# Optimization experiments

Measured on AMD Instinct MI355X. Metric: run time of the kernel, lower is better.

## Reference

```python
import jax, jax.numpy as jnp
import numpy as np
from jax import lax

NPOINT, NSAMPLE, RADIUS = 1024, 32, 0.2
IN_CH, DIM, HEADS = 64, 128, 4


def _fps(xyz, npoint):
    """Farthest point sampling. xyz: [B,N,3] -> idx [B,npoint] (int32)."""
    B, N, _ = xyz.shape

    def step(carry, _):
        dist, farthest = carry
        centroid = jnp.take_along_axis(xyz, farthest[:, None, None], axis=1)  # [B,1,3]
        d = jnp.sum((xyz - centroid) ** 2, axis=-1)                            # [B,N]
        dist = jnp.minimum(dist, d)
        nxt = jnp.argmax(dist, axis=-1).astype(jnp.int32)
        return (dist, nxt), farthest

    init = (jnp.full((B, N), 1e10, xyz.dtype), jnp.zeros((B,), jnp.int32))
    _, idxs = lax.scan(step, init, None, length=npoint)
    return idxs.T  # [B,npoint]


def _ball_query(radius, nsample, xyz, new_xyz):
    """xyz [B,N,3], new_xyz [B,S,3] -> idx [B,S,nsample]."""
    N = xyz.shape[1]
    sqr = jnp.sum((new_xyz[:, :, None, :] - xyz[:, None, :, :]) ** 2, axis=-1)  # [B,S,N]
    idx = jnp.broadcast_to(jnp.arange(N, dtype=jnp.int32), sqr.shape)
    idx = jnp.where(sqr > radius * radius, N, idx)
    idx = jnp.sort(idx, axis=-1)[..., :nsample]
    first = idx[..., :1]  # center itself always within radius -> valid
    return jnp.where(idx == N, first, idx)


_gather = jax.vmap(lambda a, i: a[i])  # a [N,C], i [S,K] -> [S,K,C]


def _forward(xyz, points, Wc, bc, gamma, beta, mean, var, Wq, Wk, Wv, Wo, Wp, bp):
    xyz_n = xyz.transpose(0, 2, 1)    # [B,N,3]
    pts = points.transpose(0, 2, 1)   # [B,N,D]

    fidx = _fps(xyz_n, NPOINT)                                         # [B,S]
    new_xyz = jnp.take_along_axis(xyz_n, fidx[:, :, None], axis=1)     # [B,S,3]
    gidx = _ball_query(RADIUS, NSAMPLE, xyz_n, new_xyz)                # [B,S,K]

    grouped_xyz = _gather(xyz_n, gidx)                                 # [B,S,K,3]
    rel = grouped_xyz - new_xyz[:, :, None, :]
    grouped_pts = _gather(pts, gidx)                                   # [B,S,K,D]
    feat = jnp.concatenate([rel, grouped_pts], axis=-1)                # [B,S,K,3+D]

    # 1x1 Conv2d + BatchNorm (inference form with running stats)
    h = jnp.einsum('bskc,dc->bskd', feat, Wc) + bc
    h = (h - mean) * gamma * lax.rsqrt(var + 1e-5) + beta              # [B,S,K,DIM]

    # local transformer: xyz positional encoding + MHSA over the K neighbors
    pos = jnp.einsum('bskc,cd->bskd', grouped_xyz, Wp) + bp
    x = h + pos
    B, S, K, D = x.shape
    hd = D // HEADS
    q = (x @ Wq).reshape(B, S, K, HEADS, hd)
    k = (x @ Wk).reshape(B, S, K, HEADS, hd)
    v = (x @ Wv).reshape(B, S, K, HEADS, hd)
    attn = jax.nn.softmax(jnp.einsum('bsqhd,bskhd->bshqk', q, k) * (hd ** -0.5), axis=-1)
    o = jnp.einsum('bshqk,bskhd->bsqhd', attn, v).reshape(B, S, K, D)
    out = x + o @ Wo                                                   # [B,S,K,DIM]

    new_points = jnp.max(out, axis=2).transpose(0, 2, 1)               # [B,DIM,S]
    return new_xyz.transpose(0, 2, 1), new_points


def setup_inputs() -> dict:
    key = jax.random.key(0)
    ks = jax.random.split(key, 9)
    C = IN_CH + 3
    s = lambda k, shp: (jax.random.normal(k, shp, jnp.float32) * 0.02)
    return dict(
        xyz=jax.random.uniform(ks[0], (8, 3, 4096), jnp.float32),
        points=jax.random.normal(ks[1], (8, IN_CH, 4096), jnp.float32),
        Wc=s(ks[2], (DIM, C)), bc=jnp.zeros((DIM,), jnp.float32),
        gamma=jnp.ones((DIM,), jnp.float32), beta=jnp.zeros((DIM,), jnp.float32),
        mean=jnp.zeros((DIM,), jnp.float32), var=jnp.ones((DIM,), jnp.float32),
        Wq=s(ks[3], (DIM, DIM)), Wk=s(ks[4], (DIM, DIM)),
        Wv=s(ks[5], (DIM, DIM)), Wo=s(ks[6], (DIM, DIM)),
        Wp=s(ks[7], (3, DIM)), bp=jnp.zeros((DIM,), jnp.float32),
    )


def reference(xyz, points, Wc, bc, gamma, beta, mean, var, Wq, Wk, Wv, Wo, Wp, bp):
    return _forward(xyz, points, Wc, bc, gamma, beta, mean, var, Wq, Wk, Wv, Wo, Wp, bp)
```

## Files before the change

kernel.cpp:

```cpp
#include <hip/hip_runtime.h>
#include <math.h>

#define B 8
#define N 4096
#define S 1024
#define K 32
#define CIN 64
#define DIM 128
#define NH 4
#define HD 32
#define PTROW 68
#define NT_BLOCKS 256

typedef __attribute__((ext_vector_type(8))) short bfrag;
typedef __attribute__((ext_vector_type(4))) float f32x4;

#define MFMA(a, b, c) __builtin_amdgcn_mfma_f32_16x16x32_bf16((a), (b), (c), 0, 0, 0)

__device__ __forceinline__ unsigned short f2bf(float f) {
    union { float f; unsigned u; } v; v.f = f;
    unsigned r = v.u + 0x7FFFu + ((v.u >> 16) & 1u);
    return (unsigned short)(r >> 16);
}

#define DPPMAXF(var, CTRL) {                                                              \
    int _o = __builtin_amdgcn_update_dpp(__float_as_int(var), __float_as_int(var),        \
                                         CTRL, 0xf, 0xf, false);                          \
    var = fmaxf(var, __int_as_float(_o));                                                 \
}
#define DPPMINU(var, CTRL) {                                                              \
    unsigned _o = (unsigned)__builtin_amdgcn_update_dpp((int)(var), (int)(var),           \
                                                        CTRL, 0xf, 0xf, false);          \
    var = (_o < (var)) ? _o : (var);                                                      \
}

__global__ __launch_bounds__(256) void k_mega(
    const float* __restrict__ xyz, const float* __restrict__ points,
    const float* __restrict__ Wc, const float* __restrict__ bc,
    const float* __restrict__ gamma, const float* __restrict__ beta,
    const float* __restrict__ mean, const float* __restrict__ var,
    const float* __restrict__ Wp, const float* __restrict__ bp,
    const float* __restrict__ Wq, const float* __restrict__ Wk,
    const float* __restrict__ Wv, const float* __restrict__ Wo,
    float* __restrict__ ptsT, float* __restrict__ nxyz, float* __restrict__ out_xyz,
    unsigned short* __restrict__ WF, float* __restrict__ biasv) {
    __shared__ float pxyz[N * 3];
    __shared__ float cent[S * 3];
    __shared__ __align__(16) unsigned long long wbuf[2][4];
    const int tid = threadIdx.x;
    int blk = blockIdx.x;

    if (blk < 8) {
        const int b = blk;
        const float* X = xyz + (size_t)b * 3 * N;
        float px[16], py[16], pz[16], pd[16];
#pragma unroll
        for (int i = 0; i < 16; i++) {
            int n = tid + i * 256;
            px[i] = X[n]; py[i] = X[N + n]; pz[i] = X[2 * N + n];
            pxyz[n * 3 + 0] = px[i];
            pxyz[n * 3 + 1] = py[i];
            pxyz[n * 3 + 2] = pz[i];
            pd[i] = 1e10f;
        }
        __syncthreads();
        float cx = pxyz[0], cy = pxyz[1], cz = pxyz[2];

        for (int t = 0; t < S; t++) {
            if (tid == 0) { cent[t * 3] = cx; cent[t * 3 + 1] = cy; cent[t * 3 + 2] = cz; }
            if (t == S - 1) break;

            float bv = -1.0f; int slot = 0;
#pragma unroll
            for (int i = 0; i < 16; i++) {
                float dx = px[i] - cx, dy = py[i] - cy, dz = pz[i] - cz;
                float d = __fadd_rn(__fadd_rn(__fmul_rn(dx, dx), __fmul_rn(dy, dy)), __fmul_rn(dz, dz));
                float pn = fminf(pd[i], d);
                pd[i] = pn;
                bool gt = pn > bv;
                bv = gt ? pn : bv;
                slot = gt ? i : slot;
            }
            float m = bv;
            DPPMAXF(m, 0x111)
            DPPMAXF(m, 0x112)
            DPPMAXF(m, 0x114)
            DPPMAXF(m, 0x118)
            DPPMAXF(m, 0x142)
            DPPMAXF(m, 0x143)
            float wmax = __int_as_float(__builtin_amdgcn_readlane(__float_as_int(m), 63));
            unsigned bi = (unsigned)(tid + (slot << 8));
            unsigned bic = (bv == wmax) ? bi : 0xFFFFFFFFu;
            DPPMINU(bic, 0x111)
            DPPMINU(bic, 0x112)
            DPPMINU(bic, 0x114)
            DPPMINU(bic, 0x118)
            DPPMINU(bic, 0x142)
            DPPMINU(bic, 0x143)
            if ((tid & 63) == 63) {
                unsigned long long key =
                    ((unsigned long long)__float_as_uint(wmax) << 32) | (0xFFFFFFFFu - bic);
                wbuf[t & 1][tid >> 6] = key;
            }
            __syncthreads();
            ulonglong2 ab = *(const ulonglong2*)&wbuf[t & 1][0];
            ulonglong2 cd = *(const ulonglong2*)&wbuf[t & 1][2];
            unsigned long long kA = ab.x > ab.y ? ab.x : ab.y;
            unsigned long long kB = cd.x > cd.y ? cd.x : cd.y;
            unsigned long long km = kA > kB ? kA : kB;
            int best = (int)(0xFFFFFFFFu - (unsigned)km);
            cx = pxyz[best * 3]; cy = pxyz[best * 3 + 1]; cz = pxyz[best * 3 + 2];
        }
        __syncthreads();
        for (int i = tid; i < S; i += 256) {
            float a = cent[i * 3], c1 = cent[i * 3 + 1], c2 = cent[i * 3 + 2];
            nxyz[(b * S + i) * 3 + 0] = a;
            nxyz[(b * S + i) * 3 + 1] = c1;
            nxyz[(b * S + i) * 3 + 2] = c2;
            out_xyz[b * 3 * S + i] = a;
            out_xyz[b * 3 * S + S + i] = c1;
            out_xyz[b * 3 * S + 2 * S + i] = c2;
        }
        return;
    }
    blk -= 8;
    if (blk < NT_BLOCKS) {
        const int total = B * N * PTROW;
        for (int idx = blk * 256 + tid; idx < total; idx += NT_BLOCKS * 256) {
            int c = idx % PTROW;
            int n = (idx / PTROW) % N;
            int b = idx / (PTROW * N);
            float v = 0.0f;
            if (c < 3) v = xyz[(b * 3 + c) * N + n];
            else if (c < 67) v = points[(b * CIN + (c - 3)) * N + n];
            ptsT[idx] = v;
        }
        return;
    }
    blk -= NT_BLOCKS;
    if (blk < 19) {
        int mat, kt, base;
        if (blk < 3) { mat = 0; kt = blk; base = 0; }
        else { mat = 1 + (blk - 3) / 4; kt = (blk - 3) % 4; base = 12288 + (mat - 1) * 16384; }
        const float* W = (mat == 1) ? Wq : (mat == 2) ? Wk : (mat == 3) ? Wv : Wo;
        const int lane = tid & 63;
#pragma unroll
        for (int g2 = 0; g2 < 2; g2++) {
            int gnt = (tid >> 6) * 2 + g2;
            int n = gnt * 16 + (lane & 15);
            int k0 = kt * 32 + (lane >> 4) * 8;
            unsigned short* dst = WF + base + (size_t)((kt * 8 + gnt) * 64 + lane) * 8;
            float a = (mat == 0) ? (gamma[n] / sqrtf(var[n] + 1e-5f)) : 0.0f;
#pragma unroll
            for (int i = 0; i < 8; i++) {
                int k = k0 + i;
                float v;
                if (mat == 0) v = (k < 67) ? Wc[n * 67 + k] * a : (k < 70) ? Wp[(k - 67) * 128 + n] : 0.0f;
                else v = W[k * 128 + n];
                dst[i] = f2bf(v);
            }
        }
        return;
    }
    if (tid < DIM) {
        float a = gamma[tid] / sqrtf(var[tid] + 1e-5f);
        biasv[tid] = bc[tid] * a + beta[tid] - mean[tid] * a + bp[tid];
    }
}

__global__ void k_ball(const float* __restrict__ xyz, const float* __restrict__ nxyz,
                       int* __restrict__ gidx) {
    const int g = blockIdx.x * 4 + (threadIdx.x >> 6);
    const int lane = threadIdx.x & 63;
    const int b = g >> 10;
    const float* X = xyz + (size_t)b * 3 * N;
    float cx = nxyz[g * 3 + 0], cy = nxyz[g * 3 + 1], cz = nxyz[g * 3 + 2];
    int cnt = 0;
    int first = -1;
    for (int base = 0; base < N && cnt < K; base += 64) {
        int n = base + lane;
        float dx = cx - X[n], dy = cy - X[N + n], dz = cz - X[2 * N + n];
        float d = __fadd_rn(__fadd_rn(__fmul_rn(dx, dx), __fmul_rn(dy, dy)), __fmul_rn(dz, dz));
        bool in = (d <= 0.04f);
        unsigned long long m = __ballot(in);
        int pre = __popcll(m & ((1ull << lane) - 1ull));
        if (in && cnt + pre < K) gidx[g * K + cnt + pre] = n;
        if (first < 0 && m) first = base + (int)__ffsll((unsigned long long)m) - 1;
        cnt += __popcll(m);
    }
    if (cnt < K) {
        for (int i = cnt + lane; i < K; i += 64) gidx[g * K + i] = first;
    }
}

#define LDS_X   0
#define LDS_A   8192
#define LDS_K   16384
#define LDS_VT  24576
#define LDS_MISC 38912
#define LDS_TOTAL 39056

#define LDSA_READ(off, row, colb) \
    (*(const bfrag*)(smem + (off) + ((row) << 8) + ((colb) ^ (((row) & 7) << 4))))
#define LDS_ST16(off, row, colb, val) \
    (*(unsigned short*)(smem + (off) + ((row) << 8) + ((colb) ^ (((row) & 7) << 4))) = (val))

__global__ __launch_bounds__(256, 4) void k_group(
    const float* __restrict__ ptsT, const float* __restrict__ nxyz,
    const int* __restrict__ gidx, const unsigned short* __restrict__ WF,
    const float* __restrict__ bias, float* __restrict__ outp) {
    __shared__ __align__(16) char smem[LDS_TOTAL];
    const int g = blockIdx.x, b = g >> 10, s = g & 1023;
    const int tid = threadIdx.x;
    const int w = tid >> 6, l = tid & 63;
    const int lane16 = l & 15, lquad = l >> 4;
    const int ncol = w * 32;

    int* nidx = (int*)(smem + LDS_MISC);
    float* ctr = (float*)(smem + LDS_MISC + 128);

    if (tid < K) nidx[tid] = gidx[g * K + tid];
    if (tid >= 64 && tid < 67) ctr[tid - 64] = nxyz[g * 3 + (tid - 64)];
    for (int i = tid; i < 32 * 32; i += 256) {
        int p = i >> 5, c = 64 + (i & 31);
        LDS_ST16(LDS_A, p, c * 2, (unsigned short)0);
    }
    __syncthreads();

    {
        const int p = tid >> 3, j = tid & 7;
        const float* src = ptsT + (size_t)(b * N + nidx[p]) * PTROW;
        float c0 = ctr[0], c1 = ctr[1], c2 = ctr[2];
        for (int c = j; c < 70; c += 8) {
            float v;
            if (c < 3) v = src[c] - (c == 0 ? c0 : c == 1 ? c1 : c2);
            else if (c < 67) v = src[c];
            else v = src[c - 67];
            LDS_ST16(LDS_A, p, c * 2, f2bf(v));
        }
    }
    __syncthreads();

    f32x4 accx[2][2];
    {
        float bv0 = bias[ncol + lane16], bv1 = bias[ncol + 16 + lane16];
        accx[0][0] = f32x4{bv0, bv0, bv0, bv0}; accx[1][0] = accx[0][0];
        accx[0][1] = f32x4{bv1, bv1, bv1, bv1}; accx[1][1] = accx[0][1];
        const bfrag* WallF = (const bfrag*)WF;
#pragma unroll
        for (int kt = 0; kt < 3; kt++) {
            bfrag a0 = LDSA_READ(LDS_A, lane16, kt * 64 + lquad * 16);
            bfrag a1 = LDSA_READ(LDS_A, 16 + lane16, kt * 64 + lquad * 16);
            bfrag b0 = WallF[(kt * 8 + w * 2 + 0) * 64 + l];
            bfrag b1 = WallF[(kt * 8 + w * 2 + 1) * 64 + l];
            accx[0][0] = MFMA(a0, b0, accx[0][0]);
            accx[0][1] = MFMA(a0, b1, accx[0][1]);
            accx[1][0] = MFMA(a1, b0, accx[1][0]);
            accx[1][1] = MFMA(a1, b1, accx[1][1]);
        }
#pragma unroll
        for (int mt = 0; mt < 2; mt++)
#pragma unroll
            for (int nt = 0; nt < 2; nt++)
#pragma unroll
                for (int r = 0; r < 4; r++)
                    LDS_ST16(LDS_X, mt * 16 + lquad * 4 + r, (ncol + nt * 16 + lane16) * 2,
                             f2bf(accx[mt][nt][r]));
    }
    __syncthreads();

    {
        const bfrag* WQF = (const bfrag*)(WF + 12288);
        const bfrag* WKF = (const bfrag*)(WF + 28672);
        const bfrag* WVF = (const bfrag*)(WF + 45056);
#pragma unroll
        for (int m = 0; m < 3; m++) {
            const bfrag* BW = (m == 0) ? WQF : (m == 1) ? WKF : WVF;
            f32x4 acc[2][2] = {};
#pragma unroll
            for (int kt = 0; kt < 4; kt++) {
                bfrag a0 = LDSA_READ(LDS_X, lane16, kt * 64 + lquad * 16);
                bfrag a1 = LDSA_READ(LDS_X, 16 + lane16, kt * 64 + lquad * 16);
                bfrag b0 = BW[(kt * 8 + w * 2 + 0) * 64 + l];
                bfrag b1 = BW[(kt * 8 + w * 2 + 1) * 64 + l];
                acc[0][0] = MFMA(a0, b0, acc[0][0]);
                acc[0][1] = MFMA(a0, b1, acc[0][1]);
                acc[1][0] = MFMA(a1, b0, acc[1][0]);
                acc[1][1] = MFMA(a1, b1, acc[1][1]);
            }
            if (m < 2) {
                int dst = (m == 0) ? LDS_A : LDS_K;
#pragma unroll
                for (int mt = 0; mt < 2; mt++)
#pragma unroll
                    for (int nt = 0; nt < 2; nt++)
#pragma unroll
                        for (int r = 0; r < 4; r++)
                            LDS_ST16(dst, mt * 16 + lquad * 4 + r, (ncol + nt * 16 + lane16) * 2,
                                     f2bf(acc[mt][nt][r]));
            } else {
#pragma unroll
                for (int mt = 0; mt < 2; mt++)
#pragma unroll
                    for (int nt = 0; nt < 2; nt++)
#pragma unroll
                        for (int r = 0; r < 4; r++) {
                            int d = ncol + nt * 16 + lane16;
                            int j = mt * 16 + lquad * 4 + r;
                            *(unsigned short*)(smem + LDS_VT + d * 112 + j * 2) = f2bf(acc[mt][nt][r]);
                        }
            }
        }
    }
    __syncthreads();

    {
        const int h = w;
        const int hb = h * 64;
        bfrag aq0 = LDSA_READ(LDS_A, lane16, hb + lquad * 16);
        bfrag aq1 = LDSA_READ(LDS_A, 16 + lane16, hb + lquad * 16);
        bfrag bk0 = LDSA_READ(LDS_K, lane16, hb + lquad * 16);
        bfrag bk1 = LDSA_READ(LDS_K, 16 + lane16, hb + lquad * 16);
        f32x4 sc[2][2] = {};
        sc[0][0] = MFMA(aq0, bk0, sc[0][0]);
        sc[0][1] = MFMA(aq0, bk1, sc[0][1]);
        sc[1][0] = MFMA(aq1, bk0, sc[1][0]);
        sc[1][1] = MFMA(aq1, bk1, sc[1][1]);

        const float scale = 0.17677669529663687f;
        float p_[2][2][4];
        float mx[2][4], sm[2][4];
#pragma unroll
        for (int mt = 0; mt < 2; mt++)
#pragma unroll
            for (int r = 0; r < 4; r++) {
                p_[mt][0][r] = sc[mt][0][r] * scale;
                p_[mt][1][r] = sc[mt][1][r] * scale;
                mx[mt][r] = fmaxf(p_[mt][0][r], p_[mt][1][r]);
            }
#pragma unroll
        for (int d = 1; d < 16; d <<= 1)
#pragma unroll
            for (int mt = 0; mt < 2; mt++)
#pragma unroll
                for (int r = 0; r < 4; r++)
                    mx[mt][r] = fmaxf(mx[mt][r], __shfl_xor(mx[mt][r], d));
#pragma unroll
        for (int mt = 0; mt < 2; mt++)
#pragma unroll
            for (int r = 0; r < 4; r++) {
                float e0 = __expf(p_[mt][0][r] - mx[mt][r]);
                float e1 = __expf(p_[mt][1][r] - mx[mt][r]);
                p_[mt][0][r] = e0; p_[mt][1][r] = e1;
                sm[mt][r] = e0 + e1;
            }
#pragma unroll
        for (int d = 1; d < 16; d <<= 1)
#pragma unroll
            for (int mt = 0; mt < 2; mt++)
#pragma unroll
                for (int r = 0; r < 4; r++)
                    sm[mt][r] += __shfl_xor(sm[mt][r], d);
#pragma unroll
        for (int mt = 0; mt < 2; mt++)
#pragma unroll
            for (int r = 0; r < 4; r++) {
                float inv = 1.0f / sm[mt][r];
                int row = mt * 16 + lquad * 4 + r;
                LDS_ST16(LDS_X, row, (h * 32 + lane16) * 2, f2bf(p_[mt][0][r] * inv));
                LDS_ST16(LDS_X, row, (h * 32 + 16 + lane16) * 2, f2bf(p_[mt][1][r] * inv));
            }

        f32x4 oacc[2][2] = {};
        bfrag ap0 = LDSA_READ(LDS_X, lane16, hb + lquad * 16);
        bfrag ap1 = LDSA_READ(LDS_X, 16 + lane16, hb + lquad * 16);
        bfrag bv0 = *(const bfrag*)(smem + LDS_VT + (h * 32 + lane16) * 112 + lquad * 16);
        bfrag bv1 = *(const bfrag*)(smem + LDS_VT + (h * 32 + 16 + lane16) * 112 + lquad * 16);
        oacc[0][0] = MFMA(ap0, bv0, oacc[0][0]);
        oacc[0][1] = MFMA(ap0, bv1, oacc[0][1]);
        oacc[1][0] = MFMA(ap1, bv0, oacc[1][0]);
        oacc[1][1] = MFMA(ap1, bv1, oacc[1][1]);
#pragma unroll
        for (int mt = 0; mt < 2; mt++)
#pragma unroll
            for (int nt = 0; nt < 2; nt++)
#pragma unroll
                for (int r = 0; r < 4; r++)
                    LDS_ST16(LDS_A, mt * 16 + lquad * 4 + r, (h * 32 + nt * 16 + lane16) * 2,
                             f2bf(oacc[mt][nt][r]));
    }
    __syncthreads();

    {
        const bfrag* WOF = (const bfrag*)(WF + 61440);
        f32x4 acc[2][2];
#pragma unroll
        for (int mt = 0; mt < 2; mt++)
#pragma unroll
            for (int nt = 0; nt < 2; nt++) acc[mt][nt] = accx[mt][nt];
#pragma unroll
        for (int kt = 0; kt < 4; kt++) {
            bfrag a0 = LDSA_READ(LDS_A, lane16, kt * 64 + lquad * 16);
            bfrag a1 = LDSA_READ(LDS_A, 16 + lane16, kt * 64 + lquad * 16);
            bfrag b0 = WOF[(kt * 8 + w * 2 + 0) * 64 + l];
            bfrag b1 = WOF[(kt * 8 + w * 2 + 1) * 64 + l];
            acc[0][0] = MFMA(a0, b0, acc[0][0]);
            acc[0][1] = MFMA(a0, b1, acc[0][1]);
            acc[1][0] = MFMA(a1, b0, acc[1][0]);
            acc[1][1] = MFMA(a1, b1, acc[1][1]);
        }
        float mnt[2];
#pragma unroll
        for (int nt = 0; nt < 2; nt++) {
            float m = acc[0][nt][0];
#pragma unroll
            for (int r = 1; r < 4; r++) m = fmaxf(m, acc[0][nt][r]);
#pragma unroll
            for (int r = 0; r < 4; r++) m = fmaxf(m, acc[1][nt][r]);
            m = fmaxf(m, __shfl_xor(m, 16));
            m = fmaxf(m, __shfl_xor(m, 32));
            mnt[nt] = m;
        }
        if (lquad == 0) {
#pragma unroll
            for (int nt = 0; nt < 2; nt++) {
                int d = ncol + nt * 16 + lane16;
                outp[((size_t)b * DIM + d) * S + s] = mnt[nt];
            }
        }
    }
}

extern "C" void kernel_launch(void* const* d_in, const int* in_sizes, int n_in,
                              void* d_out, int out_size, void* d_ws, size_t ws_size,
                              hipStream_t stream) {
    const float* xyz = (const float*)d_in[0];
    const float* points = (const float*)d_in[1];
    const float* Wc = (const float*)d_in[2];
    const float* bc = (const float*)d_in[3];
    const float* gamma = (const float*)d_in[4];
    const float* beta = (const float*)d_in[5];
    const float* mean = (const float*)d_in[6];
    const float* var = (const float*)d_in[7];
    const float* Wq = (const float*)d_in[8];
    const float* Wk = (const float*)d_in[9];
    const float* Wv = (const float*)d_in[10];
    const float* Wo = (const float*)d_in[11];
    const float* Wp = (const float*)d_in[12];
    const float* bp = (const float*)d_in[13];

    float* out_xyz = (float*)d_out;
    float* out_pts = out_xyz + B * 3 * S;

    char* ws = (char*)d_ws;
    float* ptsT = (float*)ws;
    size_t off = (size_t)B * N * PTROW * 4;
    float* nxyz = (float*)(ws + off); off += (size_t)B * S * 3 * 4;
    int* gidxp = (int*)(ws + off); off += (size_t)B * S * K * 4;
    unsigned short* WF = (unsigned short*)(ws + off); off += 77824 * 2;
    float* biasv = (float*)(ws + off); off += DIM * 4;

    k_mega<<<8 + NT_BLOCKS + 19 + 1, 256, 0, stream>>>(
        xyz, points, Wc, bc, gamma, beta, mean, var, Wp, bp, Wq, Wk, Wv, Wo,
        ptsT, nxyz, out_xyz, WF, biasv);
    k_ball<<<B * S / 4, 256, 0, stream>>>(xyz, nxyz, gidxp);
    k_group<<<B * S, 256, 0, stream>>>(ptsT, nxyz, gidxp, WF, biasv, out_pts);
}
```

Baseline: 772.0 us.

## Fuse FPS, ball query and grouping into persistent kernel with streaming flags

Merges the three kernels into one persistent launch. Eight blocks run farthest point sampling and publish centroids in chunks of 16 through release atomics and per-batch flags. The remaining 504 worker blocks first do the transpose and weight packing, meet at a grid-wide barrier, then loop over groups, spinning until their centroid is published. Each worker does the ball query inline, so group processing overlaps with the serial FPS and the gidx round trip disappears. In exchange it relies on every block being co-resident, uses spin-waits, and raises LDS use per block, which can lower occupancy.

```diff
diff --git a/kernel.cpp b/kernel.cpp
--- a/kernel.cpp
+++ b/kernel.cpp
@@ -7,10 +7,8 @@
 #define K 32
 #define CIN 64
 #define DIM 128
-#define NH 4
-#define HD 32
 #define PTROW 68
-#define NT_BLOCKS 256
+#define NWORK 504
 
 typedef __attribute__((ext_vector_type(8))) short bfrag;
 typedef __attribute__((ext_vector_type(4))) float f32x4;
@@ -34,7 +32,19 @@
     var = (_o < (var)) ? _o : (var);                                                      \
 }
 
-__global__ __launch_bounds__(256) void k_mega(
+#define LDS_X   0
+#define LDS_A   8192
+#define LDS_K   16384
+#define LDS_VT  24576
+#define LDS_MISC 38912
+#define SMEM_TOTAL 61952
+
+#define LDSA_READ(off, row, colb) \
+    (*(const bfrag*)(smem + (off) + ((row) << 8) + ((colb) ^ (((row) & 7) << 4))))
+#define LDS_ST16(off, row, colb, val) \
+    (*(unsigned short*)(smem + (off) + ((row) << 8) + ((colb) ^ (((row) & 7) << 4))) = (val))
+
+__global__ __launch_bounds__(256) void k_fused(
     const float* __restrict__ xyz, const float* __restrict__ points,
     const float* __restrict__ Wc, const float* __restrict__ bc,
     const float* __restrict__ gamma, const float* __restrict__ beta,
@@ -42,32 +52,42 @@
     const float* __restrict__ Wp, const float* __restrict__ bp,
     const float* __restrict__ Wq, const float* __restrict__ Wk,
     const float* __restrict__ Wv, const float* __restrict__ Wo,
-    float* __restrict__ ptsT, float* __restrict__ nxyz, float* __restrict__ out_xyz,
-    unsigned short* __restrict__ WF, float* __restrict__ biasv) {
-    __shared__ float pxyz[N * 3];
-    __shared__ float cent[S * 3];
-    __shared__ __align__(16) unsigned long long wbuf[2][4];
+    float* __restrict__ ptsT, float* nxyz, float* __restrict__ out_xyz,
+    unsigned short* __restrict__ WF, float* __restrict__ biasv,
+    int* flags, int* tdone, float* __restrict__ outp) {
+    __shared__ __align__(16) char smem[SMEM_TOTAL];
     const int tid = threadIdx.x;
-    int blk = blockIdx.x;
+    const int blk = blockIdx.x;
 
     if (blk < 8) {
         const int b = blk;
         const float* X = xyz + (size_t)b * 3 * N;
+        float* xs = (float*)smem;
+        float* ys = (float*)(smem + 16384);
+        float* zs = (float*)(smem + 32768);
+        float* cent = (float*)(smem + 49152);
+        unsigned long long* wbuf = (unsigned long long*)(smem + 61440);
+
         float px[16], py[16], pz[16], pd[16];
 #pragma unroll
         for (int i = 0; i < 16; i++) {
             int n = tid + i * 256;
             px[i] = X[n]; py[i] = X[N + n]; pz[i] = X[2 * N + n];
-            pxyz[n * 3 + 0] = px[i];
-            pxyz[n * 3 + 1] = py[i];
-            pxyz[n * 3 + 2] = pz[i];
+            xs[n] = px[i]; ys[n] = py[i]; zs[n] = pz[i];
             pd[i] = 1e10f;
         }
         __syncthreads();
-        float cx = pxyz[0], cy = pxyz[1], cz = pxyz[2];
+        float cx = xs[0], cy = ys[0], cz = zs[0];
 
         for (int t = 0; t < S; t++) {
             if (tid == 0) { cent[t * 3] = cx; cent[t * 3 + 1] = cy; cent[t * 3 + 2] = cz; }
+            const bool pub = (t != 0) && ((t & 15) == 0);
+            if (pub && tid < 48) {
+                int row = t - 16 + tid / 3, c = tid % 3;
+                __hip_atomic_store((unsigned*)&nxyz[((size_t)b * S + row) * 3 + c],
+                                   __float_as_uint(cent[row * 3 + c]),
+                                   __ATOMIC_RELEASE, __HIP_MEMORY_SCOPE_AGENT);
+            }
             if (t == S - 1) break;
 
             float bv = -1.0f; int slot = 0;
@@ -89,44 +109,50 @@
             DPPMAXF(m, 0x142)
             DPPMAXF(m, 0x143)
             float wmax = __int_as_float(__builtin_amdgcn_readlane(__float_as_int(m), 63));
-            unsigned bi = (unsigned)(tid + (slot << 8));
-            unsigned bic = (bv == wmax) ? bi : 0xFFFFFFFFu;
-            DPPMINU(bic, 0x111)
-            DPPMINU(bic, 0x112)
-            DPPMINU(bic, 0x114)
-            DPPMINU(bic, 0x118)
-            DPPMINU(bic, 0x142)
-            DPPMINU(bic, 0x143)
-            if ((tid & 63) == 63) {
-                unsigned long long key =
-                    ((unsigned long long)__float_as_uint(wmax) << 32) | (0xFFFFFFFFu - bic);
-                wbuf[t & 1][tid >> 6] = key;
-            }
+            unsigned cand = (bv == wmax) ? (unsigned)(tid + (slot << 8)) : 0xFFFFFFFFu;
+            DPPMINU(cand, 0x111)
+            DPPMINU(cand, 0x112)
+            DPPMINU(cand, 0x114)
+            DPPMINU(cand, 0x118)
+            DPPMINU(cand, 0x142)
+            DPPMINU(cand, 0x143)
+            if ((tid & 63) == 63)
+                wbuf[(t & 1) * 4 + (tid >> 6)] =
+                    ((unsigned long long)__float_as_uint(wmax) << 32) | (0xFFFFFFFFu - cand);
             __syncthreads();
-            ulonglong2 ab = *(const ulonglong2*)&wbuf[t & 1][0];
-            ulonglong2 cd = *(const ulonglong2*)&wbuf[t & 1][2];
+            if (pub && tid == 0)
+                __hip_atomic_fetch_add(&flags[b], 16, __ATOMIC_RELEASE, __HIP_MEMORY_SCOPE_AGENT);
+            ulonglong2 ab = *(const ulonglong2*)&wbuf[(t & 1) * 4 + 0];
+            ulonglong2 cd = *(const ulonglong2*)&wbuf[(t & 1) * 4 + 2];
             unsigned long long kA = ab.x > ab.y ? ab.x : ab.y;
             unsigned long long kB = cd.x > cd.y ? cd.x : cd.y;
             unsigned long long km = kA > kB ? kA : kB;
             int best = (int)(0xFFFFFFFFu - (unsigned)km);
-            cx = pxyz[best * 3]; cy = pxyz[best * 3 + 1]; cz = pxyz[best * 3 + 2];
-        }
-        __syncthreads();
+            cx = xs[best]; cy = ys[best]; cz = zs[best];
+        }
+        __syncthreads();
+        if (tid < 48) {
+            int row = 1008 + tid / 3, c = tid % 3;
+            __hip_atomic_store((unsigned*)&nxyz[((size_t)b * S + row) * 3 + c],
+                               __float_as_uint(cent[row * 3 + c]),
+                               __ATOMIC_RELEASE, __HIP_MEMORY_SCOPE_AGENT);
+        }
+        __syncthreads();
+        if (tid == 0)
+            __hip_atomic_fetch_add(&flags[b], 16, __ATOMIC_RELEASE, __HIP_MEMORY_SCOPE_AGENT);
         for (int i = tid; i < S; i += 256) {
-            float a = cent[i * 3], c1 = cent[i * 3 + 1], c2 = cent[i * 3 + 2];
-            nxyz[(b * S + i) * 3 + 0] = a;
-            nxyz[(b * S + i) * 3 + 1] = c1;
-            nxyz[(b * S + i) * 3 + 2] = c2;
-            out_xyz[b * 3 * S + i] = a;
-            out_xyz[b * 3 * S + S + i] = c1;
-            out_xyz[b * 3 * S + 2 * S + i] = c2;
+            out_xyz[b * 3 * S + i] = cent[i * 3];
+            out_xyz[b * 3 * S + S + i] = cent[i * 3 + 1];
+            out_xyz[b * 3 * S + 2 * S + i] = cent[i * 3 + 2];
         }
         return;
     }
-    blk -= 8;
-    if (blk < NT_BLOCKS) {
+
+    const int w = blk - 8;
+
+    {
         const int total = B * N * PTROW;
-        for (int idx = blk * 256 + tid; idx < total; idx += NT_BLOCKS * 256) {
+        for (int idx = w * 256 + tid; idx < total; idx += NWORK * 256) {
             int c = idx % PTROW;
             int n = (idx / PTROW) % N;
             int b = idx / (PTROW * N);
@@ -135,297 +161,288 @@
             else if (c < 67) v = points[(b * CIN + (c - 3)) * N + n];
             ptsT[idx] = v;
         }
-        return;
+        if (w < 19) {
+            int mat, kt, base;
+            if (w < 3) { mat = 0; kt = w; base = 0; }
+            else { mat = 1 + (w - 3) / 4; kt = (w - 3) % 4; base = 12288 + (mat - 1) * 16384; }
+            const float* W = (mat == 1) ? Wq : (mat == 2) ? Wk : (mat == 3) ? Wv : Wo;
+            const int lane = tid & 63;
+#pragma unroll
+            for (int g2 = 0; g2 < 2; g2++) {
+                int gnt = (tid >> 6) * 2 + g2;
+                int n = gnt * 16 + (lane & 15);
+                int k0 = kt * 32 + (lane >> 4) * 8;
+                unsigned short* dst = WF + base + (size_t)((kt * 8 + gnt) * 64 + lane) * 8;
+                float a = (mat == 0) ? (gamma[n] / sqrtf(var[n] + 1e-5f)) : 0.0f;
+#pragma unroll
+                for (int i = 0; i < 8; i++) {
+                    int k = k0 + i;
+                    float v;
+                    if (mat == 0) v = (k < 67) ? Wc[n * 67 + k] * a : (k < 70) ? Wp[(k - 67) * 128 + n] : 0.0f;
+                    else v = W[k * 128 + n];
+                    dst[i] = f2bf(v);
+                }
+            }
+        }
+        if (w == 19 && tid < DIM) {
+            float a = gamma[tid] / sqrtf(var[tid] + 1e-5f);
+            biasv[tid] = bc[tid] * a + beta[tid] - mean[tid] * a + bp[tid];
+        }
     }
-    blk -= NT_BLOCKS;
-    if (blk < 19) {
-        int mat, kt, base;
-        if (blk < 3) { mat = 0; kt = blk; base = 0; }
-        else { mat = 1 + (blk - 3) / 4; kt = (blk - 3) % 4; base = 12288 + (mat - 1) * 16384; }
-        const float* W = (mat == 1) ? Wq : (mat == 2) ? Wk : (mat == 3) ? Wv : Wo;
-        const int lane = tid & 63;
-#pragma unroll
-        for (int g2 = 0; g2 < 2; g2++) {
-            int gnt = (tid >> 6) * 2 + g2;
-            int n = gnt * 16 + (lane & 15);
-            int k0 = kt * 32 + (lane >> 4) * 8;
-            unsigned short* dst = WF + base + (size_t)((kt * 8 + gnt) * 64 + lane) * 8;
-            float a = (mat == 0) ? (gamma[n] / sqrtf(var[n] + 1e-5f)) : 0.0f;
-#pragma unroll
-            for (int i = 0; i < 8; i++) {
-                int k = k0 + i;
-                float v;
-                if (mat == 0) v = (k < 67) ? Wc[n * 67 + k] * a : (k < 70) ? Wp[(k - 67) * 128 + n] : 0.0f;
-                else v = W[k * 128 + n];
-                dst[i] = f2bf(v);
-            }
-        }
-        return;
+    __threadfence();
+    __syncthreads();
+    if (tid == 0) {
+        __hip_atomic_fetch_add(tdone, 1, __ATOMIC_RELEASE, __HIP_MEMORY_SCOPE_AGENT);
+        while (__hip_atomic_load(tdone, __ATOMIC_ACQUIRE, __HIP_MEMORY_SCOPE_AGENT) < NWORK)
+            __builtin_amdgcn_s_sleep(2);
     }
-    if (tid < DIM) {
-        float a = gamma[tid] / sqrtf(var[tid] + 1e-5f);
-        biasv[tid] = bc[tid] * a + beta[tid] - mean[tid] * a + bp[tid];
-    }
-}
-
-__global__ void k_ball(const float* __restrict__ xyz, const float* __restrict__ nxyz,
-                       int* __restrict__ gidx) {
-    const int g = blockIdx.x * 4 + (threadIdx.x >> 6);
-    const int lane = threadIdx.x & 63;
-    const int b = g >> 10;
-    const float* X = xyz + (size_t)b * 3 * N;
-    float cx = nxyz[g * 3 + 0], cy = nxyz[g * 3 + 1], cz = nxyz[g * 3 + 2];
-    int cnt = 0;
-    int first = -1;
-    for (int base = 0; base < N && cnt < K; base += 64) {
-        int n = base + lane;
-        float dx = cx - X[n], dy = cy - X[N + n], dz = cz - X[2 * N + n];
-        float d = __fadd_rn(__fadd_rn(__fmul_rn(dx, dx), __fmul_rn(dy, dy)), __fmul_rn(dz, dz));
-        bool in = (d <= 0.04f);
-        unsigned long long m = __ballot(in);
-        int pre = __popcll(m & ((1ull << lane) - 1ull));
-        if (in && cnt + pre < K) gidx[g * K + cnt + pre] = n;
-        if (first < 0 && m) first = base + (int)__ffsll((unsigned long long)m) - 1;
-        cnt += __popcll(m);
-    }
-    if (cnt < K) {
-        for (int i = cnt + lane; i < K; i += 64) gidx[g * K + i] = first;
-    }
-}
-
-#define LDS_X   0
-#define LDS_A   8192
-#define LDS_K   16384
-#define LDS_VT  24576
-#define LDS_MISC 38912
-#define LDS_TOTAL 39056
-
-#define LDSA_READ(off, row, colb) \
-    (*(const bfrag*)(smem + (off) + ((row) << 8) + ((colb) ^ (((row) & 7) << 4))))
-#define LDS_ST16(off, row, colb, val) \
-    (*(unsigned short*)(smem + (off) + ((row) << 8) + ((colb) ^ (((row) & 7) << 4))) = (val))
-
-__global__ __launch_bounds__(256, 4) void k_group(
-    const float* __restrict__ ptsT, const float* __restrict__ nxyz,
-    const int* __restrict__ gidx, const unsigned short* __restrict__ WF,
-    const float* __restrict__ bias, float* __restrict__ outp) {
-    __shared__ __align__(16) char smem[LDS_TOTAL];
-    const int g = blockIdx.x, b = g >> 10, s = g & 1023;
-    const int tid = threadIdx.x;
-    const int w = tid >> 6, l = tid & 63;
+    __syncthreads();
+
+    const int wv = tid >> 6, l = tid & 63;
     const int lane16 = l & 15, lquad = l >> 4;
-    const int ncol = w * 32;
-
+    const int ncol = wv * 32;
     int* nidx = (int*)(smem + LDS_MISC);
     float* ctr = (float*)(smem + LDS_MISC + 128);
 
-    if (tid < K) nidx[tid] = gidx[g * K + tid];
-    if (tid >= 64 && tid < 67) ctr[tid - 64] = nxyz[g * 3 + (tid - 64)];
-    for (int i = tid; i < 32 * 32; i += 256) {
-        int p = i >> 5, c = 64 + (i & 31);
-        LDS_ST16(LDS_A, p, c * 2, (unsigned short)0);
-    }
-    __syncthreads();
-
-    {
-        const int p = tid >> 3, j = tid & 7;
-        const float* src = ptsT + (size_t)(b * N + nidx[p]) * PTROW;
-        float c0 = ctr[0], c1 = ctr[1], c2 = ctr[2];
-        for (int c = j; c < 70; c += 8) {
-            float v;
-            if (c < 3) v = src[c] - (c == 0 ? c0 : c == 1 ? c1 : c2);
-            else if (c < 67) v = src[c];
-            else v = src[c - 67];
-            LDS_ST16(LDS_A, p, c * 2, f2bf(v));
-        }
-    }
-    __syncthreads();
-
-    f32x4 accx[2][2];
-    {
-        float bv0 = bias[ncol + lane16], bv1 = bias[ncol + 16 + lane16];
-        accx[0][0] = f32x4{bv0, bv0, bv0, bv0}; accx[1][0] = accx[0][0];
-        accx[0][1] = f32x4{bv1, bv1, bv1, bv1}; accx[1][1] = accx[0][1];
-        const bfrag* WallF = (const bfrag*)WF;
-#pragma unroll
-        for (int kt = 0; kt < 3; kt++) {
-            bfrag a0 = LDSA_READ(LDS_A, lane16, kt * 64 + lquad * 16);
-            bfrag a1 = LDSA_READ(LDS_A, 16 + lane16, kt * 64 + lquad * 16);
-            bfrag b0 = WallF[(kt * 8 + w * 2 + 0) * 64 + l];
-            bfrag b1 = WallF[(kt * 8 + w * 2 + 1) * 64 + l];
-            accx[0][0] = MFMA(a0, b0, accx[0][0]);
-            accx[0][1] = MFMA(a0, b1, accx[0][1]);
-            accx[1][0] = MFMA(a1, b0, accx[1][0]);
-            accx[1][1] = MFMA(a1, b1, accx[1][1]);
-        }
-#pragma unroll
-        for (int mt = 0; mt < 2; mt++)
-#pragma unroll
-            for (int nt = 0; nt < 2; nt++)
-#pragma unroll
-                for (int r = 0; r < 4; r++)
-                    LDS_ST16(LDS_X, mt * 16 + lquad * 4 + r, (ncol + nt * 16 + lane16) * 2,
-                             f2bf(accx[mt][nt][r]));
-    }
-    __syncthreads();
-
-    {
-        const bfrag* WQF = (const bfrag*)(WF + 12288);
-        const bfrag* WKF = (const bfrag*)(WF + 28672);
-        const bfrag* WVF = (const bfrag*)(WF + 45056);
-#pragma unroll
-        for (int m = 0; m < 3; m++) {
-            const bfrag* BW = (m == 0) ? WQF : (m == 1) ? WKF : WVF;
-            f32x4 acc[2][2] = {};
+    for (int g = w; g < B * S; g += NWORK) {
+        const int s = g >> 3, b = g & 7;
+        if (tid == 0) {
+            while (__hip_atomic_load(&flags[b], __ATOMIC_ACQUIRE, __HIP_MEMORY_SCOPE_AGENT) <= s)
+                __builtin_amdgcn_s_sleep(2);
+        }
+        __syncthreads();
+
+        if (tid < 64) {
+            float cx = __uint_as_float(__hip_atomic_load((unsigned*)&nxyz[((size_t)b * S + s) * 3 + 0],
+                                                         __ATOMIC_RELAXED, __HIP_MEMORY_SCOPE_AGENT));
+            float cy = __uint_as_float(__hip_atomic_load((unsigned*)&nxyz[((size_t)b * S + s) * 3 + 1],
+                                                         __ATOMIC_RELAXED, __HIP_MEMORY_SCOPE_AGENT));
+            float cz = __uint_as_float(__hip_atomic_load((unsigned*)&nxyz[((size_t)b * S + s) * 3 + 2],
+                                                         __ATOMIC_RELAXED, __HIP_MEMORY_SCOPE_AGENT));
+            if (tid == 0) { ctr[0] = cx; ctr[1] = cy; ctr[2] = cz; }
+            const float* X = xyz + (size_t)b * 3 * N;
+            int cnt = 0, first = -1;
+            for (int base = 0; base < N && cnt < K; base += 64) {
+                int n = base + tid;
+                float dx = cx - X[n], dy = cy - X[N + n], dz = cz - X[2 * N + n];
+                float d = __fadd_rn(__fadd_rn(__fmul_rn(dx, dx), __fmul_rn(dy, dy)), __fmul_rn(dz, dz));
+                bool in = (d <= 0.04f);
+                unsigned long long mm = __ballot(in);
+                int pre = __popcll(mm & ((1ull << tid) - 1ull));
+                if (in && cnt + pre < K) nidx[cnt + pre] = n;
+                if (first < 0 && mm) first = base + (int)__ffsll((unsigned long long)mm) - 1;
+                cnt += __popcll(mm);
+            }
+            if (cnt < K) {
+                for (int i = cnt + tid; i < K; i += 64) nidx[i] = first;
+            }
+        }
+        for (int i = tid; i < 32 * 32; i += 256) {
+            int p = i >> 5, c = 64 + (i & 31);
+            LDS_ST16(LDS_A, p, c * 2, (unsigned short)0);
+        }
+        __syncthreads();
+
+        {
+            const int p = tid >> 3, j = tid & 7;
+            const float* src = ptsT + (size_t)(b * N + nidx[p]) * PTROW;
+            float c0 = ctr[0], c1 = ctr[1], c2 = ctr[2];
+            for (int c = j; c < 70; c += 8) {
+                float v;
+                if (c < 3) v = src[c] - (c == 0 ? c0 : c == 1 ? c1 : c2);
+                else if (c < 67) v = src[c];
+                else v = src[c - 67];
+                LDS_ST16(LDS_A, p, c * 2, f2bf(v));
+            }
+        }
+        __syncthreads();
+
+        f32x4 accx[2][2];
+        {
+            float bv0 = biasv[ncol + lane16], bv1 = biasv[ncol + 16 + lane16];
+            accx[0][0] = f32x4{bv0, bv0, bv0, bv0}; accx[1][0] = accx[0][0];
+            accx[0][1] = f32x4{bv1, bv1, bv1, bv1}; accx[1][1] = accx[0][1];
+            const bfrag* WallF = (const bfrag*)WF;
+#pragma unroll
+            for (int kt = 0; kt < 3; kt++) {
+                bfrag a0 = LDSA_READ(LDS_A, lane16, kt * 64 + lquad * 16);
+                bfrag a1 = LDSA_READ(LDS_A, 16 + lane16, kt * 64 + lquad * 16);
+                bfrag b0 = WallF[(kt * 8 + wv * 2 + 0) * 64 + l];
+                bfrag b1 = WallF[(kt * 8 + wv * 2 + 1) * 64 + l];
+                accx[0][0] = MFMA(a0, b0, accx[0][0]);
+                accx[0][1] = MFMA(a0, b1, accx[0][1]);
+                accx[1][0] = MFMA(a1, b0, accx[1][0]);
+                accx[1][1] = MFMA(a1, b1, accx[1][1]);
+            }
+#pragma unroll
+            for (int mt = 0; mt < 2; mt++)
+#pragma unroll
+                for (int nt = 0; nt < 2; nt++)
+#pragma unroll
+                    for (int r = 0; r < 4; r++)
+                        LDS_ST16(LDS_X, mt * 16 + lquad * 4 + r, (ncol + nt * 16 + lane16) * 2,
+                                 f2bf(accx[mt][nt][r]));
+        }
+        __syncthreads();
+
+        {
+            const bfrag* WQF = (const bfrag*)(WF + 12288);
+            const bfrag* WKF = (const bfrag*)(WF + 28672);
+            const bfrag* WVF = (const bfrag*)(WF + 45056);
+#pragma unroll
+            for (int m = 0; m < 3; m++) {
+                const bfrag* BW = (m == 0) ? WQF : (m == 1) ? WKF : WVF;
+                f32x4 acc[2][2] = {};
+#pragma unroll
+                for (int kt = 0; kt < 4; kt++) {
+                    bfrag a0 = LDSA_READ(LDS_X, lane16, kt * 64 + lquad * 16);
+                    bfrag a1 = LDSA_READ(LDS_X, 16 + lane16, kt * 64 + lquad * 16);
+                    bfrag b0 = BW[(kt * 8 + wv * 2 + 0) * 64 + l];
+                    bfrag b1 = BW[(kt * 8 + wv * 2 + 1) * 64 + l];
+                    acc[0][0] = MFMA(a0, b0, acc[0][0]);
+                    acc[0][1] = MFMA(a0, b1, acc[0][1]);
+                    acc[1][0] = MFMA(a1, b0, acc[1][0]);
+                    acc[1][1] = MFMA(a1, b1, acc[1][1]);
+                }
+                if (m < 2) {
+                    int dst = (m == 0) ? LDS_A : LDS_K;
+#pragma unroll
+                    for (int mt = 0; mt < 2; mt++)
+#pragma unroll
+                        for (int nt = 0; nt < 2; nt++)
+#pragma unroll
+                            for (int r = 0; r < 4; r++)
+                                LDS_ST16(dst, mt * 16 + lquad * 4 + r, (ncol + nt * 16 + lane16) * 2,
+                                         f2bf(acc[mt][nt][r]));
+                } else {
+#pragma unroll
+                    for (int mt = 0; mt < 2; mt++)
+#pragma unroll
+                        for (int nt = 0; nt < 2; nt++)
+#pragma unroll
+                            for (int r = 0; r < 4; r++) {
+                                int d = ncol + nt * 16 + lane16;
+                                int j = mt * 16 + lquad * 4 + r;
+                                *(unsigned short*)(smem + LDS_VT + d * 112 + j * 2) = f2bf(acc[mt][nt][r]);
+                            }
+                }
+            }
+        }
+        __syncthreads();
+
+        {
+            const int h = wv;
+            const int hb = h * 64;
+            bfrag aq0 = LDSA_READ(LDS_A, lane16, hb + lquad * 16);
+            bfrag aq1 = LDSA_READ(LDS_A, 16 + lane16, hb + lquad * 16);
+            bfrag bk0 = LDSA_READ(LDS_K, lane16, hb + lquad * 16);
+            bfrag bk1 = LDSA_READ(LDS_K, 16 + lane16, hb + lquad * 16);
+            f32x4 sc[2][2] = {};
+            sc[0][0] = MFMA(aq0, bk0, sc[0][0]);
+            sc[0][1] = MFMA(aq0, bk1, sc[0][1]);
+            sc[1][0] = MFMA(aq1, bk0, sc[1][0]);
+            sc[1][1] = MFMA(aq1, bk1, sc[1][1]);
+
+            const float scale = 0.17677669529663687f;
+            float p_[2][2][4];
+            float mx[2][4], sm[2][4];
+#pragma unroll
+            for (int mt = 0; mt < 2; mt++)
+#pragma unroll
+                for (int r = 0; r < 4; r++) {
+                    p_[mt][0][r] = sc[mt][0][r] * scale;
+                    p_[mt][1][r] = sc[mt][1][r] * scale;
+                    mx[mt][r] = fmaxf(p_[mt][0][r], p_[mt][1][r]);
+                }
+#pragma unroll
+            for (int d = 1; d < 16; d <<= 1)
+#pragma unroll
+                for (int mt = 0; mt < 2; mt++)
+#pragma unroll
+                    for (int r = 0; r < 4; r++)
+                        mx[mt][r] = fmaxf(mx[mt][r], __shfl_xor(mx[mt][r], d));
+#pragma unroll
+            for (int mt = 0; mt < 2; mt++)
+#pragma unroll
+                for (int r = 0; r < 4; r++) {
+                    float e0 = __expf(p_[mt][0][r] - mx[mt][r]);
+                    float e1 = __expf(p_[mt][1][r] - mx[mt][r]);
+                    p_[mt][0][r] = e0; p_[mt][1][r] = e1;
+                    sm[mt][r] = e0 + e1;
+                }
+#pragma unroll
+            for (int d = 1; d < 16; d <<= 1)
+#pragma unroll
+                for (int mt = 0; mt < 2; mt++)
+#pragma unroll
+                    for (int r = 0; r < 4; r++)
+                        sm[mt][r] += __shfl_xor(sm[mt][r], d);
+#pragma unroll
+            for (int mt = 0; mt < 2; mt++)
+#pragma unroll
+                for (int r = 0; r < 4; r++) {
+                    float inv = 1.0f / sm[mt][r];
+                    int row = mt * 16 + lquad * 4 + r;
+                    LDS_ST16(LDS_X, row, (h * 32 + lane16) * 2, f2bf(p_[mt][0][r] * inv));
+                    LDS_ST16(LDS_X, row, (h * 32 + 16 + lane16) * 2, f2bf(p_[mt][1][r] * inv));
+                }
+
+            f32x4 oacc[2][2] = {};
+            bfrag ap0 = LDSA_READ(LDS_X, lane16, hb + lquad * 16);
+            bfrag ap1 = LDSA_READ(LDS_X, 16 + lane16, hb + lquad * 16);
+            bfrag bv0 = *(const bfrag*)(smem + LDS_VT + (h * 32 + lane16) * 112 + lquad * 16);
+            bfrag bv1 = *(const bfrag*)(smem + LDS_VT + (h * 32 + 16 + lane16) * 112 + lquad * 16);
+            oacc[0][0] = MFMA(ap0, bv0, oacc[0][0]);
+            oacc[0][1] = MFMA(ap0, bv1, oacc[0][1]);
+            oacc[1][0] = MFMA(ap1, bv0, oacc[1][0]);
+            oacc[1][1] = MFMA(ap1, bv1, oacc[1][1]);
+#pragma unroll
+            for (int mt = 0; mt < 2; mt++)
+#pragma unroll
+                for (int nt = 0; nt < 2; nt++)
+#pragma unroll
+                    for (int r = 0; r < 4; r++)
+                        LDS_ST16(LDS_A, mt * 16 + lquad * 4 + r, (h * 32 + nt * 16 + lane16) * 2,
+                                 f2bf(oacc[mt][nt][r]));
+        }
+        __syncthreads();
+
+        {
+            const bfrag* WOF = (const bfrag*)(WF + 61440);
+            f32x4 acc[2][2];
+#pragma unroll
+            for (int mt = 0; mt < 2; mt++)
+#pragma unroll
+                for (int nt = 0; nt < 2; nt++) acc[mt][nt] = accx[mt][nt];
 #pragma unroll
             for (int kt = 0; kt < 4; kt++) {
-                bfrag a0 = LDSA_READ(LDS_X, lane16, kt * 64 + lquad * 16);
-                bfrag a1 = LDSA_READ(LDS_X, 16 + lane16, kt * 64 + lquad * 16);
-                bfrag b0 = BW[(kt * 8 + w * 2 + 0) * 64 + l];
-                bfrag b1 = BW[(kt * 8 + w * 2 + 1) * 64 + l];
+                bfrag a0 = LDSA_READ(LDS_A, lane16, kt * 64 + lquad * 16);
+                bfrag a1 = LDSA_READ(LDS_A, 16 + lane16, kt * 64 + lquad * 16);
+                bfrag b0 = WOF[(kt * 8 + wv * 2 + 0) * 64 + l];
+                bfrag b1 = WOF[(kt * 8 + wv * 2 + 1) * 64 + l];
                 acc[0][0] = MFMA(a0, b0, acc[0][0]);
                 acc[0][1] = MFMA(a0, b1, acc[0][1]);
                 acc[1][0] = MFMA(a1, b0, acc[1][0]);
                 acc[1][1] = MFMA(a1, b1, acc[1][1]);
             }
-            if (m < 2) {
-                int dst = (m == 0) ? LDS_A : LDS_K;
-#pragma unroll
-                for (int mt = 0; mt < 2; mt++)
-#pragma unroll
-                    for (int nt = 0; nt < 2; nt++)
-#pragma unroll
-                        for (int r = 0; r < 4; r++)
-                            LDS_ST16(dst, mt * 16 + lquad * 4 + r, (ncol + nt * 16 + lane16) * 2,
-                                     f2bf(acc[mt][nt][r]));
-            } else {
-#pragma unroll
-                for (int mt = 0; mt < 2; mt++)
-#pragma unroll
-                    for (int nt = 0; nt < 2; nt++)
-#pragma unroll
-                        for (int r = 0; r < 4; r++) {
-                            int d = ncol + nt * 16 + lane16;
-                            int j = mt * 16 + lquad * 4 + r;
-                            *(unsigned short*)(smem + LDS_VT + d * 112 + j * 2) = f2bf(acc[mt][nt][r]);
-                        }
-            }
-        }
-    }
-    __syncthreads();
-
-    {
-        const int h = w;
-        const int hb = h * 64;
-        bfrag aq0 = LDSA_READ(LDS_A, lane16, hb + lquad * 16);
-        bfrag aq1 = LDSA_READ(LDS_A, 16 + lane16, hb + lquad * 16);
-        bfrag bk0 = LDSA_READ(LDS_K, lane16, hb + lquad * 16);
-        bfrag bk1 = LDSA_READ(LDS_K, 16 + lane16, hb + lquad * 16);
-        f32x4 sc[2][2] = {};
-        sc[0][0] = MFMA(aq0, bk0, sc[0][0]);
-        sc[0][1] = MFMA(aq0, bk1, sc[0][1]);
-        sc[1][0] = MFMA(aq1, bk0, sc[1][0]);
-        sc[1][1] = MFMA(aq1, bk1, sc[1][1]);
-
-        const float scale = 0.17677669529663687f;
-        float p_[2][2][4];
-        float mx[2][4], sm[2][4];
-#pragma unroll
-        for (int mt = 0; mt < 2; mt++)
-#pragma unroll
-            for (int r = 0; r < 4; r++) {
-                p_[mt][0][r] = sc[mt][0][r] * scale;
-                p_[mt][1][r] = sc[mt][1][r] * scale;
-                mx[mt][r] = fmaxf(p_[mt][0][r], p_[mt][1][r]);
-            }
-#pragma unroll
-        for (int d = 1; d < 16; d <<= 1)
-#pragma unroll
-            for (int mt = 0; mt < 2; mt++)
-#pragma unroll
-                for (int r = 0; r < 4; r++)
-                    mx[mt][r] = fmaxf(mx[mt][r], __shfl_xor(mx[mt][r], d));
-#pragma unroll
-        for (int mt = 0; mt < 2; mt++)
-#pragma unroll
-            for (int r = 0; r < 4; r++) {
-                float e0 = __expf(p_[mt][0][r] - mx[mt][r]);
-                float e1 = __expf(p_[mt][1][r] - mx[mt][r]);
-                p_[mt][0][r] = e0; p_[mt][1][r] = e1;
-                sm[mt][r] = e0 + e1;
-            }
-#pragma unroll
-        for (int d = 1; d < 16; d <<= 1)
-#pragma unroll
-            for (int mt = 0; mt < 2; mt++)
-#pragma unroll
-                for (int r = 0; r < 4; r++)
-                    sm[mt][r] += __shfl_xor(sm[mt][r], d);
-#pragma unroll
-        for (int mt = 0; mt < 2; mt++)
-#pragma unroll
-            for (int r = 0; r < 4; r++) {
-                float inv = 1.0f / sm[mt][r];
-                int row = mt * 16 + lquad * 4 + r;
-                LDS_ST16(LDS_X, row, (h * 32 + lane16) * 2, f2bf(p_[mt][0][r] * inv));
-                LDS_ST16(LDS_X, row, (h * 32 + 16 + lane16) * 2, f2bf(p_[mt][1][r] * inv));
-            }
-
-        f32x4 oacc[2][2] = {};
-        bfrag ap0 = LDSA_READ(LDS_X, lane16, hb + lquad * 16);
-        bfrag ap1 = LDSA_READ(LDS_X, 16 + lane16, hb + lquad * 16);
-        bfrag bv0 = *(const bfrag*)(smem + LDS_VT + (h * 32 + lane16) * 112 + lquad * 16);
-        bfrag bv1 = *(const bfrag*)(smem + LDS_VT + (h * 32 + 16 + lane16) * 112 + lquad * 16);
-        oacc[0][0] = MFMA(ap0, bv0, oacc[0][0]);
-        oacc[0][1] = MFMA(ap0, bv1, oacc[0][1]);
-        oacc[1][0] = MFMA(ap1, bv0, oacc[1][0]);
-        oacc[1][1] = MFMA(ap1, bv1, oacc[1][1]);
-#pragma unroll
-        for (int mt = 0; mt < 2; mt++)
-#pragma unroll
-            for (int nt = 0; nt < 2; nt++)
-#pragma unroll
-                for (int r = 0; r < 4; r++)
-                    LDS_ST16(LDS_A, mt * 16 + lquad * 4 + r, (h * 32 + nt * 16 + lane16) * 2,
-                             f2bf(oacc[mt][nt][r]));
-    }
-    __syncthreads();
-
-    {
-        const bfrag* WOF = (const bfrag*)(WF + 61440);
-        f32x4 acc[2][2];
-#pragma unroll
-        for (int mt = 0; mt < 2; mt++)
-#pragma unroll
-            for (int nt = 0; nt < 2; nt++) acc[mt][nt] = accx[mt][nt];
-#pragma unroll
-        for (int kt = 0; kt < 4; kt++) {
-            bfrag a0 = LDSA_READ(LDS_A, lane16, kt * 64 + lquad * 16);
-            bfrag a1 = LDSA_READ(LDS_A, 16 + lane16, kt * 64 + lquad * 16);
-            bfrag b0 = WOF[(kt * 8 + w * 2 + 0) * 64 + l];
-            bfrag b1 = WOF[(kt * 8 + w * 2 + 1) * 64 + l];
-            acc[0][0] = MFMA(a0, b0, acc[0][0]);
-            acc[0][1] = MFMA(a0, b1, acc[0][1]);
-            acc[1][0] = MFMA(a1, b0, acc[1][0]);
-            acc[1][1] = MFMA(a1, b1, acc[1][1]);
-        }
-        float mnt[2];
-#pragma unroll
-        for (int nt = 0; nt < 2; nt++) {
-            float m = acc[0][nt][0];
-#pragma unroll
-            for (int r = 1; r < 4; r++) m = fmaxf(m, acc[0][nt][r]);
-#pragma unroll
-            for (int r = 0; r < 4; r++) m = fmaxf(m, acc[1][nt][r]);
-            m = fmaxf(m, __shfl_xor(m, 16));
-            m = fmaxf(m, __shfl_xor(m, 32));
-            mnt[nt] = m;
-        }
-        if (lquad == 0) {
+            float mnt[2];
 #pragma unroll
             for (int nt = 0; nt < 2; nt++) {
-                int d = ncol + nt * 16 + lane16;
-                outp[((size_t)b * DIM + d) * S + s] = mnt[nt];
+                float m = acc[0][nt][0];
+#pragma unroll
+                for (int r = 1; r < 4; r++) m = fmaxf(m, acc[0][nt][r]);
+#pragma unroll
+                for (int r = 0; r < 4; r++) m = fmaxf(m, acc[1][nt][r]);
+                m = fmaxf(m, __shfl_xor(m, 16));
+                m = fmaxf(m, __shfl_xor(m, 32));
+                mnt[nt] = m;
+            }
+            if (lquad == 0) {
+#pragma unroll
+                for (int nt = 0; nt < 2; nt++) {
+                    int d = ncol + nt * 16 + lane16;
+                    outp[((size_t)b * DIM + d) * S + s] = mnt[nt];
+                }
             }
         }
     }
@@ -456,13 +473,14 @@
     float* ptsT = (float*)ws;
     size_t off = (size_t)B * N * PTROW * 4;
     float* nxyz = (float*)(ws + off); off += (size_t)B * S * 3 * 4;
-    int* gidxp = (int*)(ws + off); off += (size_t)B * S * K * 4;
     unsigned short* WF = (unsigned short*)(ws + off); off += 77824 * 2;
     float* biasv = (float*)(ws + off); off += DIM * 4;
-
-    k_mega<<<8 + NT_BLOCKS + 19 + 1, 256, 0, stream>>>(
+    off = (off + 255) & ~(size_t)255;
+    int* flags = (int*)(ws + off);
+    int* tdone = flags + 8;
+
+    hipMemsetAsync(flags, 0, 64, stream);
+    k_fused<<<8 + NWORK, 256, 0, stream>>>(
         xyz, points, Wc, bc, gamma, beta, mean, var, Wp, bp, Wq, Wk, Wv, Wo,
-        ptsT, nxyz, out_xyz, WF, biasv);
-    k_ball<<<B * S / 4, 256, 0, stream>>>(xyz, nxyz, gidxp);
-    k_group<<<B * S, 256, 0, stream>>>(ptsT, nxyz, gidxp, WF, biasv, out_pts);
+        ptsT, nxyz, out_xyz, WF, biasv, flags, tdone, out_pts);
 }
```

Result: slower. 850.3 us (+10.2%).
